# Performance work log

Hardware: AMD Instinct MI355X
Metric: run time of the kernel (lower is better)

The kernel has to match this reference:

```python
import jax, jax.numpy as jnp
import numpy as np

B = 262144       # batch
M = 128          # manifold_dim
Q = M // 4       # quaternions per sample


def setup_inputs() -> dict:
    key = jax.random.key(0)
    ks = jax.random.split(key, 8)
    return {
        "vision_ycbcr": jax.random.normal(ks[0], (B, 3), jnp.float32),
        "text_bytes": jax.random.randint(ks[1], (B, 1), 0, 256, jnp.int32),
        "Wv": jax.random.normal(ks[2], (M, 3), jnp.float32) * 0.1,
        "bv": jnp.zeros((M,), jnp.float32),
        "Wt": jax.random.normal(ks[3], (M, 1), jnp.float32) * 0.1,
        "bt": jnp.zeros((M,), jnp.float32),
        "Wd": jax.random.normal(ks[4], (2, M), jnp.float32) * 0.1,
        "bd": jnp.zeros((2,), jnp.float32),
    }


def _project_to_su2(x):
    # [B, M] -> [B, Q, 4] unit quaternions
    q = x.reshape(x.shape[0], -1, 4)
    n = jnp.linalg.norm(q, axis=-1, keepdims=True) + 1e-8
    return q / n


def _karcher_flow(mods, n_iters=5):
    # mods: [K, B, Q, 4] unit quaternions on S^3; Karcher (Frechet) mean via log/exp maps
    b = mods.mean(0)
    b = b / (jnp.linalg.norm(b, axis=-1, keepdims=True) + 1e-8)
    for _ in range(n_iters):
        dot = jnp.clip(jnp.sum(mods * b, axis=-1), -1.0 + 1e-6, 1.0 - 1e-6)  # [K,B,Q]
        theta = jnp.arccos(dot)
        perp = mods - dot[..., None] * b
        pn = jnp.linalg.norm(perp, axis=-1, keepdims=True) + 1e-8
        tangent = (theta[..., None] * perp / pn).mean(0)  # [B,Q,4] mean log-map
        tn = jnp.linalg.norm(tangent, axis=-1, keepdims=True)
        b = jnp.cos(tn) * b + jnp.sin(tn) * tangent / (tn + 1e-8)  # exp map
        b = b / (jnp.linalg.norm(b, axis=-1, keepdims=True) + 1e-8)
    return b


def _eta(S):
    # eta = (1/pi) * arg(det(S)); det is real so arg is pi for det<0 else 0
    det = jnp.linalg.det(S)  # [B]
    ang = jnp.where(det < 0, jnp.pi, 0.0)
    return ang / jnp.pi


def reference(vision_ycbcr, text_bytes, Wv, bv, Wt, bt, Wd, bd):
    v_atoms = vision_ycbcr @ Wv.T + bv                       # [B, M]
    t_atoms = text_bytes.astype(jnp.float32) @ Wt.T + bt     # [B, M]
    v_man = _project_to_su2(v_atoms)                          # [B, Q, 4]
    t_man = _project_to_su2(t_atoms)
    mods = jnp.stack([v_man, t_man], axis=0)                  # [2, B, Q, 4]
    bary_q = _karcher_flow(mods)                              # [B, Q, 4]
    barycenter = bary_q.reshape(bary_q.shape[0], -1)          # [B, M]
    s_v = v_man[:, ::8, :]    # [B, 4, 4]
    s_t = t_man[:, ::8, :]
    s_b = bary_q[:, ::8, :]
    eta_v = _eta(s_v)
    eta_t = _eta(s_t)
    eta_b = _eta(s_b)
    logic_curvature = jnp.abs(eta_v - eta_t).mean()
    iso_loss = jnp.linalg.norm(eta_v - eta_b) + jnp.linalg.norm(eta_t - eta_b)
    decision = barycenter @ Wd.T + bd                         # DiscreteDecisionEngine logits [B, 2]
    return (barycenter, eta_v, eta_t, eta_b, iso_loss, logic_curvature, decision)
```

## Files before the change

### kernel.cpp

```cpp
#include <hip/hip_runtime.h>
#include <math.h>

#define B_ROWS 262144
#define ROWS_PER_BLOCK 8
#define THREADS (ROWS_PER_BLOCK * 32)
#define NBLOCKS (B_ROWS / ROWS_PER_BLOCK)

#define BARY_OFF 0
#define EV_OFF   ((size_t)B_ROWS * 128)
#define ET_OFF   ((size_t)B_ROWS * 129)
#define EB_OFF   ((size_t)B_ROWS * 130)
#define ISO_OFF  ((size_t)B_ROWS * 131)
#define LC_OFF   ((size_t)B_ROWS * 131 + 1)
#define DEC_OFF  ((size_t)B_ROWS * 131 + 2)

__device__ __forceinline__ float rsq_guard(float s) {
    return __builtin_amdgcn_rsqf(fmaxf(s, 1e-14f));
}

__device__ __forceinline__ float det4(const float* m) {
    float s0 = m[0]*m[5]  - m[1]*m[4];
    float s1 = m[0]*m[6]  - m[2]*m[4];
    float s2 = m[0]*m[7]  - m[3]*m[4];
    float s3 = m[1]*m[6]  - m[2]*m[5];
    float s4 = m[1]*m[7]  - m[3]*m[5];
    float s5 = m[2]*m[7]  - m[3]*m[6];
    float c5 = m[10]*m[15] - m[11]*m[14];
    float c4 = m[9]*m[15]  - m[11]*m[13];
    float c3 = m[9]*m[14]  - m[10]*m[13];
    float c2 = m[8]*m[15]  - m[11]*m[12];
    float c1 = m[8]*m[14]  - m[10]*m[12];
    float c0 = m[8]*m[13]  - m[9]*m[12];
    return s0*c5 - s1*c4 + s2*c3 + s3*c2 - s4*c1 + s5*c0;
}

__global__ __launch_bounds__(THREADS) void bridge_main(
    const float* __restrict__ vis, const int* __restrict__ txt,
    const float* __restrict__ Wv, const float* __restrict__ bv,
    const float* __restrict__ Wt, const float* __restrict__ bt,
    const float* __restrict__ Wd, const float* __restrict__ bd,
    float* __restrict__ out, int* __restrict__ blockCnt)
{
    __shared__ float smat[ROWS_PER_BLOCK][3][16];
    __shared__ int scntP;
    const int tid = threadIdx.x;
    if (tid == 0) scntP = 0;
    const int r = tid >> 5;
    const int q = tid & 31;
    const size_t row = (size_t)blockIdx.x * ROWS_PER_BLOCK + r;

    const float x0 = vis[row*3+0], x1 = vis[row*3+1], x2 = vis[row*3+2];
    const float tx = (float)txt[row];

    float wv[12];
    ((float4*)wv)[0] = ((const float4*)Wv)[3*q+0];
    ((float4*)wv)[1] = ((const float4*)Wv)[3*q+1];
    ((float4*)wv)[2] = ((const float4*)Wv)[3*q+2];
    const float4 bv4 = ((const float4*)bv)[q];
    const float4 wt4 = ((const float4*)Wt)[q];
    const float4 bt4 = ((const float4*)bt)[q];

    float v[4], t[4], b[4];
    v[0] = fmaf(x0, wv[0], fmaf(x1, wv[1],  fmaf(x2, wv[2],  bv4.x)));
    v[1] = fmaf(x0, wv[3], fmaf(x1, wv[4],  fmaf(x2, wv[5],  bv4.y)));
    v[2] = fmaf(x0, wv[6], fmaf(x1, wv[7],  fmaf(x2, wv[8],  bv4.z)));
    v[3] = fmaf(x0, wv[9], fmaf(x1, wv[10], fmaf(x2, wv[11], bv4.w)));
    t[0] = fmaf(tx, wt4.x, bt4.x);
    t[1] = fmaf(tx, wt4.y, bt4.y);
    t[2] = fmaf(tx, wt4.z, bt4.z);
    t[3] = fmaf(tx, wt4.w, bt4.w);

    {
        const float fv = rsq_guard(v[0]*v[0]+v[1]*v[1]+v[2]*v[2]+v[3]*v[3]);
        const float ft = rsq_guard(t[0]*t[0]+t[1]*t[1]+t[2]*t[2]+t[3]*t[3]);
        #pragma unroll
        for (int j = 0; j < 4; ++j) { v[j] *= fv; t[j] *= ft; }
    }

    #pragma unroll
    for (int j = 0; j < 4; ++j) b[j] = v[j] + t[j];
    {
        const float fb = rsq_guard(b[0]*b[0]+b[1]*b[1]+b[2]*b[2]+b[3]*b[3]);
        #pragma unroll
        for (int j = 0; j < 4; ++j) b[j] *= fb;
    }

    *(float4*)(out + BARY_OFF + row * 128 + 4 * q) = make_float4(b[0], b[1], b[2], b[3]);

    const float4 wd0 = ((const float4*)Wd)[q];
    const float4 wd1 = ((const float4*)Wd)[32 + q];
    float p0 = b[0]*wd0.x + b[1]*wd0.y + b[2]*wd0.z + b[3]*wd0.w;
    float p1 = b[0]*wd1.x + b[1]*wd1.y + b[2]*wd1.z + b[3]*wd1.w;
    #pragma unroll
    for (int off = 16; off >= 1; off >>= 1) {
        p0 += __shfl_xor(p0, off, 32);
        p1 += __shfl_xor(p1, off, 32);
    }

    if ((q & 7) == 0) {
        const int k = q >> 3;
        *(float4*)&smat[r][0][k*4] = make_float4(v[0], v[1], v[2], v[3]);
        *(float4*)&smat[r][1][k*4] = make_float4(t[0], t[1], t[2], t[3]);
        *(float4*)&smat[r][2][k*4] = make_float4(b[0], b[1], b[2], b[3]);
    }
    __syncthreads();

    int e = 0;
    if (q < 3) {
        float m[16];
        const float4* mm = (const float4*)&smat[r][q][0];
        ((float4*)m)[0] = mm[0]; ((float4*)m)[1] = mm[1];
        ((float4*)m)[2] = mm[2]; ((float4*)m)[3] = mm[3];
        e = det4(m) < 0.0f ? 1 : 0;
        out[(size_t)B_ROWS * (128 + q) + row] = (float)e;
    }
    const int eV = __shfl(e, 0, 32);
    const int eT = __shfl(e, 1, 32);
    const int eB = __shfl(e, 2, 32);
    if (q == 0) {
        const int pk = (eV ^ eB) | ((eT ^ eB) << 8) | ((eV ^ eT) << 16);
        if (pk) atomicAdd(&scntP, pk);
    }
    if (q == 3) out[DEC_OFF + row*2 + 0] = p0 + bd[0];
    if (q == 4) out[DEC_OFF + row*2 + 1] = p1 + bd[1];

    __syncthreads();
    if (tid == 0) blockCnt[blockIdx.x] = scntP;
}

__global__ __launch_bounds__(1024) void bridge_finalize(
    const int* __restrict__ blockCnt, float* __restrict__ out)
{
    __shared__ int s0[16], s1[16], s2[16];
    const int tid = threadIdx.x;
    int c0 = 0, c1 = 0, c2 = 0;
    for (int i = tid; i < NBLOCKS; i += 1024) {
        const int p = blockCnt[i];
        c0 += p & 255;
        c1 += (p >> 8) & 255;
        c2 += (p >> 16) & 255;
    }
    #pragma unroll
    for (int off = 32; off >= 1; off >>= 1) {
        c0 += __shfl_down(c0, off, 64);
        c1 += __shfl_down(c1, off, 64);
        c2 += __shfl_down(c2, off, 64);
    }
    if ((tid & 63) == 0) {
        const int w = tid >> 6;
        s0[w] = c0; s1[w] = c1; s2[w] = c2;
    }
    __syncthreads();
    if (tid == 0) {
        int t0 = 0, t1 = 0, t2 = 0;
        #pragma unroll
        for (int i = 0; i < 16; ++i) { t0 += s0[i]; t1 += s1[i]; t2 += s2[i]; }
        out[ISO_OFF] = sqrtf((float)t0) + sqrtf((float)t1);
        out[LC_OFF]  = (float)t2 / (float)B_ROWS;
    }
}

extern "C" void kernel_launch(void* const* d_in, const int* in_sizes, int n_in,
                              void* d_out, int out_size, void* d_ws, size_t ws_size,
                              hipStream_t stream) {
    const float* vis = (const float*)d_in[0];
    const int*   txt = (const int*)d_in[1];
    const float* Wv  = (const float*)d_in[2];
    const float* bv  = (const float*)d_in[3];
    const float* Wt  = (const float*)d_in[4];
    const float* bt  = (const float*)d_in[5];
    const float* Wd  = (const float*)d_in[6];
    const float* bd  = (const float*)d_in[7];
    float* out = (float*)d_out;
    int* blockCnt = (int*)d_ws;

    bridge_main<<<NBLOCKS, THREADS, 0, stream>>>(vis, txt, Wv, bv, Wt, bt, Wd, bd, out, blockCnt);
    bridge_finalize<<<1, 1024, 0, stream>>>(blockCnt, out);
}
```

Measured before the change: 197.7 us.

## Loop each block over row chunks with prefetch, staged coalesced eta/decision stores

```diff
diff --git a/kernel.cpp b/kernel.cpp
--- a/kernel.cpp
+++ b/kernel.cpp
@@ -2,8 +2,10 @@
 #include <math.h>
 
 #define B_ROWS 262144
-#define ROWS_PER_BLOCK 8
-#define THREADS (ROWS_PER_BLOCK * 32)
+#define RPG 8
+#define CHUNKS 8
+#define ROWS_PER_BLOCK (RPG * CHUNKS)
+#define THREADS (RPG * 32)
 #define NBLOCKS (B_ROWS / ROWS_PER_BLOCK)
 
 #define BARY_OFF 0
@@ -13,6 +15,8 @@
 #define ISO_OFF  ((size_t)B_ROWS * 131)
 #define LC_OFF   ((size_t)B_ROWS * 131 + 1)
 #define DEC_OFF  ((size_t)B_ROWS * 131 + 2)
+
+typedef float f4 __attribute__((ext_vector_type(4)));
 
 __device__ __forceinline__ float rsq_guard(float s) {
     return __builtin_amdgcn_rsqf(fmaxf(s, 1e-14f));
@@ -41,16 +45,14 @@
     const float* __restrict__ Wd, const float* __restrict__ bd,
     float* __restrict__ out, int* __restrict__ blockCnt)
 {
-    __shared__ float smat[ROWS_PER_BLOCK][3][16];
-    __shared__ int scntP;
+    __shared__ float  smat[RPG][3][16];
+    __shared__ float  sEta[3][ROWS_PER_BLOCK];
+    __shared__ float2 sDec[ROWS_PER_BLOCK];
+    __shared__ int    spk[RPG];
+
     const int tid = threadIdx.x;
-    if (tid == 0) scntP = 0;
-    const int r = tid >> 5;
-    const int q = tid & 31;
-    const size_t row = (size_t)blockIdx.x * ROWS_PER_BLOCK + r;
-
-    const float x0 = vis[row*3+0], x1 = vis[row*3+1], x2 = vis[row*3+2];
-    const float tx = (float)txt[row];
+    const int r   = tid >> 5;
+    const int q   = tid & 31;
 
     float wv[12];
     ((float4*)wv)[0] = ((const float4*)Wv)[3*q+0];
@@ -59,83 +61,122 @@
     const float4 bv4 = ((const float4*)bv)[q];
     const float4 wt4 = ((const float4*)Wt)[q];
     const float4 bt4 = ((const float4*)bt)[q];
-
-    float v[4], t[4], b[4];
-    v[0] = fmaf(x0, wv[0], fmaf(x1, wv[1],  fmaf(x2, wv[2],  bv4.x)));
-    v[1] = fmaf(x0, wv[3], fmaf(x1, wv[4],  fmaf(x2, wv[5],  bv4.y)));
-    v[2] = fmaf(x0, wv[6], fmaf(x1, wv[7],  fmaf(x2, wv[8],  bv4.z)));
-    v[3] = fmaf(x0, wv[9], fmaf(x1, wv[10], fmaf(x2, wv[11], bv4.w)));
-    t[0] = fmaf(tx, wt4.x, bt4.x);
-    t[1] = fmaf(tx, wt4.y, bt4.y);
-    t[2] = fmaf(tx, wt4.z, bt4.z);
-    t[3] = fmaf(tx, wt4.w, bt4.w);
-
-    {
-        const float fv = rsq_guard(v[0]*v[0]+v[1]*v[1]+v[2]*v[2]+v[3]*v[3]);
-        const float ft = rsq_guard(t[0]*t[0]+t[1]*t[1]+t[2]*t[2]+t[3]*t[3]);
-        #pragma unroll
-        for (int j = 0; j < 4; ++j) { v[j] *= fv; t[j] *= ft; }
-    }
-
-    #pragma unroll
-    for (int j = 0; j < 4; ++j) b[j] = v[j] + t[j];
-    {
-        const float fb = rsq_guard(b[0]*b[0]+b[1]*b[1]+b[2]*b[2]+b[3]*b[3]);
-        #pragma unroll
-        for (int j = 0; j < 4; ++j) b[j] *= fb;
-    }
-
-    *(float4*)(out + BARY_OFF + row * 128 + 4 * q) = make_float4(b[0], b[1], b[2], b[3]);
-
     const float4 wd0 = ((const float4*)Wd)[q];
     const float4 wd1 = ((const float4*)Wd)[32 + q];
-    float p0 = b[0]*wd0.x + b[1]*wd0.y + b[2]*wd0.z + b[3]*wd0.w;
-    float p1 = b[0]*wd1.x + b[1]*wd1.y + b[2]*wd1.z + b[3]*wd1.w;
-    #pragma unroll
-    for (int off = 16; off >= 1; off >>= 1) {
-        p0 += __shfl_xor(p0, off, 32);
-        p1 += __shfl_xor(p1, off, 32);
-    }
-
-    if ((q & 7) == 0) {
-        const int k = q >> 3;
-        *(float4*)&smat[r][0][k*4] = make_float4(v[0], v[1], v[2], v[3]);
-        *(float4*)&smat[r][1][k*4] = make_float4(t[0], t[1], t[2], t[3]);
-        *(float4*)&smat[r][2][k*4] = make_float4(b[0], b[1], b[2], b[3]);
-    }
+    const float  bd0 = bd[0], bd1 = bd[1];
+
+    const size_t blockRow0 = (size_t)blockIdx.x * ROWS_PER_BLOCK;
+
+    int pkSum = 0;
+    size_t row = blockRow0 + r;
+    float x0 = vis[row*3+0], x1 = vis[row*3+1], x2 = vis[row*3+2];
+    float tx = (float)txt[row];
+
+    #pragma unroll 1
+    for (int c = 0; c < CHUNKS; ++c) {
+        const size_t nrow = (c + 1 < CHUNKS) ? (row + RPG) : row;
+        const float nx0 = vis[nrow*3+0];
+        const float nx1 = vis[nrow*3+1];
+        const float nx2 = vis[nrow*3+2];
+        const float ntx = (float)txt[nrow];
+
+        float v[4], t[4], b[4];
+        v[0] = fmaf(x0, wv[0], fmaf(x1, wv[1],  fmaf(x2, wv[2],  bv4.x)));
+        v[1] = fmaf(x0, wv[3], fmaf(x1, wv[4],  fmaf(x2, wv[5],  bv4.y)));
+        v[2] = fmaf(x0, wv[6], fmaf(x1, wv[7],  fmaf(x2, wv[8],  bv4.z)));
+        v[3] = fmaf(x0, wv[9], fmaf(x1, wv[10], fmaf(x2, wv[11], bv4.w)));
+        t[0] = fmaf(tx, wt4.x, bt4.x);
+        t[1] = fmaf(tx, wt4.y, bt4.y);
+        t[2] = fmaf(tx, wt4.z, bt4.z);
+        t[3] = fmaf(tx, wt4.w, bt4.w);
+
+        {
+            const float fv = rsq_guard(v[0]*v[0]+v[1]*v[1]+v[2]*v[2]+v[3]*v[3]);
+            const float ft = rsq_guard(t[0]*t[0]+t[1]*t[1]+t[2]*t[2]+t[3]*t[3]);
+            #pragma unroll
+            for (int j = 0; j < 4; ++j) { v[j] *= fv; t[j] *= ft; }
+        }
+
+        #pragma unroll
+        for (int j = 0; j < 4; ++j) b[j] = v[j] + t[j];
+        {
+            const float fb = rsq_guard(b[0]*b[0]+b[1]*b[1]+b[2]*b[2]+b[3]*b[3]);
+            #pragma unroll
+            for (int j = 0; j < 4; ++j) b[j] *= fb;
+        }
+
+        {
+            f4 bb; bb.x = b[0]; bb.y = b[1]; bb.z = b[2]; bb.w = b[3];
+            __builtin_nontemporal_store(bb, (f4*)(out + BARY_OFF + row * 128 + 4 * q));
+        }
+
+        float p0 = b[0]*wd0.x + b[1]*wd0.y + b[2]*wd0.z + b[3]*wd0.w;
+        float p1 = b[0]*wd1.x + b[1]*wd1.y + b[2]*wd1.z + b[3]*wd1.w;
+        #pragma unroll
+        for (int off = 16; off >= 1; off >>= 1) {
+            p0 += __shfl_xor(p0, off, 32);
+            p1 += __shfl_xor(p1, off, 32);
+        }
+
+        if ((q & 7) == 0) {
+            const int k = q >> 3;
+            *(float4*)&smat[r][0][k*4] = make_float4(v[0], v[1], v[2], v[3]);
+            *(float4*)&smat[r][1][k*4] = make_float4(t[0], t[1], t[2], t[3]);
+            *(float4*)&smat[r][2][k*4] = make_float4(b[0], b[1], b[2], b[3]);
+        }
+        __builtin_amdgcn_wave_barrier();
+
+        int e = 0;
+        if (q < 3) {
+            float m[16];
+            const float4* mm = (const float4*)&smat[r][q][0];
+            ((float4*)m)[0] = mm[0]; ((float4*)m)[1] = mm[1];
+            ((float4*)m)[2] = mm[2]; ((float4*)m)[3] = mm[3];
+            e = det4(m) < 0.0f ? 1 : 0;
+            sEta[q][c * RPG + r] = (float)e;
+        }
+        __builtin_amdgcn_wave_barrier();
+
+        const int eV = __shfl(e, 0, 32);
+        const int eT = __shfl(e, 1, 32);
+        const int eB = __shfl(e, 2, 32);
+        if (q == 0) pkSum += (eV ^ eB) | ((eT ^ eB) << 8) | ((eV ^ eT) << 16);
+        if (q == 3) sDec[c * RPG + r] = make_float2(p0 + bd0, p1 + bd1);
+
+        x0 = nx0; x1 = nx1; x2 = nx2; tx = ntx;
+        row += RPG;
+    }
+
+    if (q == 0) spk[r] = pkSum;
     __syncthreads();
 
-    int e = 0;
-    if (q < 3) {
-        float m[16];
-        const float4* mm = (const float4*)&smat[r][q][0];
-        ((float4*)m)[0] = mm[0]; ((float4*)m)[1] = mm[1];
-        ((float4*)m)[2] = mm[2]; ((float4*)m)[3] = mm[3];
-        e = det4(m) < 0.0f ? 1 : 0;
-        out[(size_t)B_ROWS * (128 + q) + row] = (float)e;
-    }
-    const int eV = __shfl(e, 0, 32);
-    const int eT = __shfl(e, 1, 32);
-    const int eB = __shfl(e, 2, 32);
-    if (q == 0) {
-        const int pk = (eV ^ eB) | ((eT ^ eB) << 8) | ((eV ^ eT) << 16);
-        if (pk) atomicAdd(&scntP, pk);
-    }
-    if (q == 3) out[DEC_OFF + row*2 + 0] = p0 + bd[0];
-    if (q == 4) out[DEC_OFF + row*2 + 1] = p1 + bd[1];
-
-    __syncthreads();
-    if (tid == 0) blockCnt[blockIdx.x] = scntP;
-}
-
-__global__ __launch_bounds__(1024) void bridge_finalize(
+    if (tid == 0) {
+        int s = 0;
+        #pragma unroll
+        for (int i = 0; i < RPG; ++i) s += spk[i];
+        blockCnt[blockIdx.x] = s;
+    }
+
+    if (tid < 192) {
+        const int s = tid >> 6, i = tid & 63;
+        __builtin_nontemporal_store(sEta[s][i],
+                                    out + (size_t)B_ROWS * (128 + s) + blockRow0 + i);
+    }
+    if (tid < 128) {
+        __builtin_nontemporal_store(((const float*)sDec)[tid],
+                                    out + DEC_OFF + blockRow0 * 2 + tid);
+    }
+}
+
+__global__ __launch_bounds__(256) void bridge_finalize(
     const int* __restrict__ blockCnt, float* __restrict__ out)
 {
-    __shared__ int s0[16], s1[16], s2[16];
+    __shared__ int s0[4], s1[4], s2[4];
     const int tid = threadIdx.x;
     int c0 = 0, c1 = 0, c2 = 0;
-    for (int i = tid; i < NBLOCKS; i += 1024) {
-        const int p = blockCnt[i];
+    #pragma unroll
+    for (int i = 0; i < NBLOCKS / 256; ++i) {
+        const int p = blockCnt[i * 256 + tid];
         c0 += p & 255;
         c1 += (p >> 8) & 255;
         c2 += (p >> 16) & 255;
@@ -154,7 +195,7 @@
     if (tid == 0) {
         int t0 = 0, t1 = 0, t2 = 0;
         #pragma unroll
-        for (int i = 0; i < 16; ++i) { t0 += s0[i]; t1 += s1[i]; t2 += s2[i]; }
+        for (int i = 0; i < 4; ++i) { t0 += s0[i]; t1 += s1[i]; t2 += s2[i]; }
         out[ISO_OFF] = sqrtf((float)t0) + sqrtf((float)t1);
         out[LC_OFF]  = (float)t2 / (float)B_ROWS;
     }
@@ -175,5 +216,5 @@
     int* blockCnt = (int*)d_ws;
 
     bridge_main<<<NBLOCKS, THREADS, 0, stream>>>(vis, txt, Wv, bv, Wt, bt, Wd, bd, out, blockCnt);
-    bridge_finalize<<<1, 1024, 0, stream>>>(blockCnt, out);
-}
+    bridge_finalize<<<1, 256, 0, stream>>>(blockCnt, out);
+}
```

New measurement: 191.7 us. 3.1% less time.
